# Optimization experiments

Measured on AMD Instinct MI355X. Metric: run time of the kernel, lower is better.

The kernel has to match this reference:

```python
import jax, jax.numpy as jnp
import numpy as np

FEAT_STRIDE = 16
PRE_NMS_TOP_N = 4000   # cfg[cfg_key].RPN_PRE_NMS_TOP_N
POST_NMS_TOP_N = 300   # cfg[cfg_key].RPN_POST_NMS_TOP_N
NMS_THRESH = 0.7       # cfg[cfg_key].RPN_NMS_THRESH


def _generate_anchors(base_size=16, ratios=(0.5, 1.0, 2.0), scales=(8, 16, 32)):
    ratios = np.array(ratios, dtype=np.float64)
    scales = np.array(scales, dtype=np.float64)
    base = np.array([1, 1, base_size, base_size], dtype=np.float64) - 1

    def whctrs(a):
        w = a[2] - a[0] + 1
        h = a[3] - a[1] + 1
        return w, h, a[0] + 0.5 * (w - 1), a[1] + 0.5 * (h - 1)

    def mk(ws, hs, xc, yc):
        ws = np.atleast_1d(ws)[:, None]
        hs = np.atleast_1d(hs)[:, None]
        return np.hstack((xc - 0.5 * (ws - 1), yc - 0.5 * (hs - 1),
                          xc + 0.5 * (ws - 1), yc + 0.5 * (hs - 1)))

    w, h, xc, yc = whctrs(base)
    size = w * h
    ws = np.round(np.sqrt(size / ratios))
    hs = np.round(ws * ratios)
    ratio_anchors = mk(ws, hs, xc, yc)
    out = []
    for i in range(ratio_anchors.shape[0]):
        w, h, xc, yc = whctrs(ratio_anchors[i])
        out.append(mk(w * scales, h * scales, xc, yc))
    return np.vstack(out).astype(np.float32)  # [9,4]


def _nms_keep(boxes, thresh):
    # boxes sorted by score desc, [N,4]; torchvision-style IoU (no +1).
    x1, y1, x2, y2 = boxes[:, 0], boxes[:, 1], boxes[:, 2], boxes[:, 3]
    areas = (x2 - x1) * (y2 - y1)
    lt = jnp.maximum(boxes[:, None, :2], boxes[None, :, :2])
    rb = jnp.minimum(boxes[:, None, 2:], boxes[None, :, 2:])
    wh = jnp.clip(rb - lt, 0.0)
    inter = wh[..., 0] * wh[..., 1]
    iou = inter / (areas[:, None] + areas[None, :] - inter + 1e-9)  # [N,N]
    N = boxes.shape[0]
    idx = jnp.arange(N)
    def body(i, keep):
        sup = (iou[i] > thresh) & (idx > i) & keep[i]
        return keep & ~sup
    return jax.lax.fori_loop(0, N, body, jnp.ones((N,), jnp.bool_))


def _per_image(boxes, scores):
    # pre-NMS top-k by score (matches sort-desc + slice)
    _, order = jax.lax.top_k(scores, PRE_NMS_TOP_N)
    b = boxes[order]
    keep = _nms_keep(jax.lax.stop_gradient(b), NMS_THRESH)
    rank = jnp.cumsum(keep) - 1                       # position among kept
    tgt = jnp.where(keep, rank, POST_NMS_TOP_N)       # OOB indices are dropped
    return jnp.zeros((POST_NMS_TOP_N, 4), boxes.dtype).at[tgt].set(b, mode='drop')


def reference(scores, bbox_deltas, im_info, anchors):
    B, A, H, W = scores.shape
    # anchor shifts over the feature grid
    sx = jnp.arange(W, dtype=scores.dtype) * FEAT_STRIDE
    sy = jnp.arange(H, dtype=scores.dtype) * FEAT_STRIDE
    yy, xx = jnp.meshgrid(sy, sx, indexing='ij')
    shifts = jnp.stack([xx.ravel(), yy.ravel(), xx.ravel(), yy.ravel()], axis=1)  # [K,4]
    all_anchors = (anchors[None, :, :] + shifts[:, None, :]).reshape(-1, 4)       # [K*A,4]

    deltas = bbox_deltas.transpose(0, 2, 3, 1).reshape(B, -1, 4)  # [B,K*A,4]
    sc = scores.transpose(0, 2, 3, 1).reshape(B, -1)              # [B,K*A]

    # bbox_transform_inv
    w = all_anchors[:, 2] - all_anchors[:, 0] + 1.0
    h = all_anchors[:, 3] - all_anchors[:, 1] + 1.0
    cx = all_anchors[:, 0] + 0.5 * w
    cy = all_anchors[:, 1] + 0.5 * h
    pcx = deltas[..., 0] * w + cx
    pcy = deltas[..., 1] * h + cy
    pw = jnp.exp(deltas[..., 2]) * w
    ph = jnp.exp(deltas[..., 3]) * h
    props = jnp.stack([pcx - 0.5 * pw, pcy - 0.5 * ph,
                       pcx + 0.5 * pw, pcy + 0.5 * ph], axis=-1)  # [B,K*A,4]

    # clip_boxes: x in [0, im_w-1], y in [0, im_h-1]
    hi = jnp.stack([im_info[:, 1] - 1, im_info[:, 0] - 1,
                    im_info[:, 1] - 1, im_info[:, 0] - 1], axis=1)  # [B,4]
    props = jnp.clip(props, 0.0, hi[:, None, :])

    boxes_out = jax.vmap(_per_image)(props, sc)  # [B,POST,4]
    batch_col = jnp.broadcast_to(
        jnp.arange(B, dtype=scores.dtype)[:, None, None], (B, POST_NMS_TOP_N, 1))
    return jnp.concatenate([batch_col, boxes_out], axis=-1)  # [B,POST,5]


def setup_inputs():
    key = jax.random.key(0)
    k1, k2 = jax.random.split(key)
    B, A, H, W = 4, 9, 50, 76
    scores = jax.random.normal(k1, (B, A, H, W), jnp.float32)
    bbox_deltas = jax.random.normal(k2, (B, 4 * A, H, W), jnp.float32) * 0.2
    im_info = jnp.tile(jnp.array([[800.0, 1216.0, 1.0]], jnp.float32), (B, 1))
    anchors = jnp.asarray(_generate_anchors())
    return {"scores": scores, "bbox_deltas": bbox_deltas,
            "im_info": im_info, "anchors": anchors}
```

## Files before the change

kernel.cpp:

```cpp
#include <hip/hip_runtime.h>
#include <stdint.h>

#define A_N 9
#define H_N 50
#define W_N 76
#define HW_N (H_N * W_N)
#define N_PROP (A_N * HW_N)
#define B_N 4
#define PRE_NMS 4000
#define POST_NMS 300
#define NMS_TH 0.7f
#define SORT_N 4096
#define MASK_WORDS 64
#define CAND_MAX 5120
#define NBINS 4096
#define NPAIR 32
#define NLW 5

__global__ __launch_bounds__(1024) void front_kernel(
    const float* __restrict__ scores,
    const float* __restrict__ deltas,
    const float* __restrict__ im_info,
    const float* __restrict__ anchors,
    float4* __restrict__ boxes,
    unsigned long long* __restrict__ keys,
    unsigned* __restrict__ cnt,
    unsigned long long* __restrict__ cand) {
#pragma clang fp contract(off)
    __shared__ unsigned hist[NBINS];
    __shared__ int Tlds;
    __shared__ unsigned cntL;
    const int b = blockIdx.x;
    const int tid = threadIdx.x;

    for (int i = tid; i < NBINS; i += 1024) hist[i] = 0u;
    if (tid == 0) cntL = 0u;
    __syncthreads();

    const float xhi = im_info[b * 3 + 1] - 1.0f;
    const float yhi = im_info[b * 3 + 0] - 1.0f;
    for (int it = 0; it < (N_PROP + 1023) / 1024; ++it) {
        int r = it * 1024 + tid;
        if (r < N_PROP) {
            int a = r / HW_N;
            int hw = r - a * HW_N;
            int hy = hw / W_N;
            int wx = hw - hy * W_N;

            float sx = (float)wx * 16.0f;
            float sy = (float)hy * 16.0f;
            float ax1 = anchors[a * 4 + 0] + sx;
            float ay1 = anchors[a * 4 + 1] + sy;
            float ax2 = anchors[a * 4 + 2] + sx;
            float ay2 = anchors[a * 4 + 3] + sy;
            float aw = ax2 - ax1 + 1.0f;
            float ah = ay2 - ay1 + 1.0f;
            float cx = ax1 + 0.5f * aw;
            float cy = ay1 + 0.5f * ah;

            const float* db = deltas + ((size_t)b * 36 + (size_t)a * 4) * HW_N + hw;
            float d0 = db[0];
            float d1 = db[HW_N];
            float d2 = db[2 * HW_N];
            float d3 = db[3 * HW_N];

            float pcx = d0 * aw + cx;
            float pcy = d1 * ah + cy;
            float pw  = expf(d2) * aw;
            float ph  = expf(d3) * ah;

            float x1 = pcx - 0.5f * pw;
            float y1 = pcy - 0.5f * ph;
            float x2 = pcx + 0.5f * pw;
            float y2 = pcy + 0.5f * ph;

            x1 = fminf(fmaxf(x1, 0.0f), xhi);
            y1 = fminf(fmaxf(y1, 0.0f), yhi);
            x2 = fminf(fmaxf(x2, 0.0f), xhi);
            y2 = fminf(fmaxf(y2, 0.0f), yhi);

            boxes[(size_t)b * N_PROP + r] = make_float4(x1, y1, x2, y2);

            float s = scores[((size_t)b * A_N + a) * HW_N + hw];
            unsigned f = __float_as_uint(s);
            unsigned sk = f ^ ((f & 0x80000000u) ? 0xFFFFFFFFu : 0x80000000u);
            unsigned n_ref = (unsigned)(hw * A_N + a);
            unsigned long long key =
                ((unsigned long long)sk << 32) | (unsigned)(~n_ref);
            keys[(size_t)b * N_PROP + r] = key;
            atomicAdd(&hist[(unsigned)(key >> 52)], 1u);
        }
    }
    __syncthreads();

    if (tid < 64) {
        int lane = tid;
        unsigned gsum = 0;
        for (int j = 0; j < 64; ++j) gsum += hist[lane * 64 + j];
        unsigned s = gsum;
        for (int d = 1; d < 64; d <<= 1) {
            unsigned t = (unsigned)__shfl_down((int)s, d);
            if (lane + d < 64) s += t;
        }
        unsigned long long bal = __ballot(s >= PRE_NMS);
        int gstar = 63 - __builtin_clzll(bal);
        unsigned after = (gstar < 63)
            ? (unsigned)__builtin_amdgcn_readlane((int)s, gstar + 1) : 0u;
        unsigned R = PRE_NMS - after;
        unsigned s2 = hist[gstar * 64 + lane];
        for (int d = 1; d < 64; d <<= 1) {
            unsigned t = (unsigned)__shfl_down((int)s2, d);
            if (lane + d < 64) s2 += t;
        }
        unsigned long long bal2 = __ballot(s2 >= R);
        int j = 63 - __builtin_clzll(bal2);
        if (lane == 0) Tlds = gstar * 64 + j;
    }
    __syncthreads();

    const int Tb = Tlds;
    for (int it = 0; it < (N_PROP + 1023) / 1024; ++it) {
        int n = it * 1024 + tid;
        bool pred = false;
        unsigned long long k = 0ull;
        if (n < N_PROP) {
            k = keys[(size_t)b * N_PROP + n];
            pred = ((int)(unsigned)(k >> 52) >= Tb);
        }
        unsigned long long m = __ballot(pred);
        if (m) {
            int lane = tid & 63;
            int lead = __ffsll((unsigned long long)m) - 1;
            unsigned base = 0;
            if (lane == lead) base = atomicAdd(&cntL, (unsigned)__popcll(m));
            base = __shfl((int)base, lead);
            if (pred) {
                unsigned pos = base + (unsigned)__popcll(m & ((1ull << lane) - 1ull));
                if (pos < CAND_MAX) cand[(size_t)b * CAND_MAX + pos] = k;
            }
        }
    }
    __syncthreads();
    if (tid == 0) cnt[b] = cntL;
}

__global__ __launch_bounds__(256) void rank_scatter_kernel(
    const unsigned long long* __restrict__ cand,
    const unsigned* __restrict__ cnt,
    const float4* __restrict__ boxes,
    float4* __restrict__ sortedBoxes) {
    __shared__ unsigned long long sk[256];
    int b = blockIdx.y;
    int tid = threadIdx.x;
    int ci = blockIdx.x * 64 + (tid >> 2);
    int q = tid & 3;
    int mc = (int)min(cnt[b], (unsigned)CAND_MAX);
    unsigned long long my = (ci < mc) ? cand[(size_t)b * CAND_MAX + ci] : 0ull;
    int rank = 0;
    int nt = (mc + 255) >> 8;
    for (int t = 0; t < nt; ++t) {
        int j = t * 256 + tid;
        sk[tid] = (j < mc) ? cand[(size_t)b * CAND_MAX + j] : 0ull;
        __syncthreads();
#pragma unroll 16
        for (int c = 0; c < 64; ++c) {
            int cc = q * 64 + ((c + q * 17) & 63);
            rank += (sk[cc] > my) ? 1 : 0;
        }
        __syncthreads();
    }
    rank += __shfl_xor(rank, 1);
    rank += __shfl_xor(rank, 2);
    if (q == 0 && ci < mc && rank < PRE_NMS) {
        unsigned n_ref = ~(unsigned)(my & 0xFFFFFFFFull);
        unsigned a = n_ref % A_N;
        unsigned hw = n_ref / A_N;
        sortedBoxes[(size_t)b * SORT_N + rank] =
            boxes[(size_t)b * N_PROP + a * HW_N + hw];
    }
    if (q == 1) {
        int pi = blockIdx.x * 64 + (tid >> 2);
        if (pi >= PRE_NMS && pi < SORT_N)
            sortedBoxes[(size_t)b * SORT_N + pi] = make_float4(0.f, 0.f, 0.f, 0.f);
    }
}

__global__ __launch_bounds__(256) void iou_mask_kernel(
    const float4* __restrict__ sortedBoxes,
    unsigned long long* __restrict__ colmaj,
    unsigned long long* __restrict__ rowmaj) {
#pragma clang fp contract(off)
    int b = blockIdx.y;
    int wv = threadIdx.x >> 6;
    int t = threadIdx.x & 63;
    int k = blockIdx.x * 4 + wv;
    int rc = 0;
    while (k >= 64 - rc) { k -= 64 - rc; ++rc; }
    int cc = rc + k;

    __shared__ float4 colb[4][64];
    colb[wv][t] = sortedBoxes[(size_t)b * SORT_N + cc * 64 + t];
    __syncthreads();

    int r = rc * 64 + t;
    float4 rb = sortedBoxes[(size_t)b * SORT_N + r];
    float rarea = (rb.z - rb.x) * (rb.w - rb.y);
    unsigned long long word = 0ull;
    for (int c = 0; c < 64; ++c) {
        int j = cc * 64 + c;
        float4 cb = colb[wv][c];
        float carea = (cb.z - cb.x) * (cb.w - cb.y);
        float ltx = fmaxf(rb.x, cb.x);
        float lty = fmaxf(rb.y, cb.y);
        float rbx = fminf(rb.z, cb.z);
        float rby = fminf(rb.w, cb.w);
        float iw = fmaxf(rbx - ltx, 0.0f);
        float ih = fmaxf(rby - lty, 0.0f);
        float inter = iw * ih;
        float iou = inter / (rarea + carea - inter + 1e-9f);
        if (iou > NMS_TH && j > r) word |= (1ull << c);
    }
    colmaj[((size_t)b * MASK_WORDS + cc) * SORT_N + r] = word;
    rowmaj[((size_t)b * SORT_N + r) * MASK_WORDS + cc] = word;
}

__device__ __forceinline__ unsigned long long rl64(unsigned long long v, int src) {
    unsigned lo = (unsigned)__builtin_amdgcn_readlane((int)(unsigned)(v & 0xFFFFFFFFull), src);
    unsigned hi = (unsigned)__builtin_amdgcn_readlane((int)(unsigned)(v >> 32), src);
    return ((unsigned long long)hi << 32) | lo;
}

__device__ __forceinline__ unsigned long long redor64(unsigned long long alive,
                                                      unsigned long long v, int lane) {
    unsigned long long x = ((alive >> lane) & 1ull) ? v : 0ull;
    x |= __shfl_xor(x, 1);
    x |= __shfl_xor(x, 2);
    x |= __shfl_xor(x, 4);
    x |= __shfl_xor(x, 8);
    x |= __shfl_xor(x, 16);
    x |= __shfl_xor(x, 32);
    return x;
}

__device__ __forceinline__ void block_sync() {
    asm volatile("s_waitcnt lgkmcnt(0)" ::: "memory");
    __builtin_amdgcn_s_barrier();
    asm volatile("" ::: "memory");
}

#define GLOAD(dst, addr) \
    asm volatile("global_load_dwordx2 %0, %1, off" : "=v"(dst) : "v"(addr))
#define WAITV0 asm volatile("s_waitcnt vmcnt(0)" ::: "memory")
#define SCHED0 __builtin_amdgcn_sched_barrier(0)

#define TILE_COL(P, t) ((t) < 6 ? 2 * (P) + (t) : 2 * (P) + 1 + ((t) - 6))
#define TILE_RB(P, t)  ((size_t)((t) < 6 ? 2 * (P) : 2 * (P) + 1) << 6)
#define TILE_ADDR(P, t) \
    (C + (size_t)(TILE_COL(P, t) < 64 ? TILE_COL(P, t) : 63) * SORT_N + TILE_RB(P, t) + lane)

#define ISSUE_PAIR(P)                                                          \
    do {                                                                       \
        pf_vmask = 0u;                                                         \
        GLOAD(pf0,  TILE_ADDR(P, 0));  if (TILE_COL(P, 0)  < 64) pf_vmask |= 1u << 0;  \
        GLOAD(pf1,  TILE_ADDR(P, 1));  if (TILE_COL(P, 1)  < 64) pf_vmask |= 1u << 1;  \
        GLOAD(pf2,  TILE_ADDR(P, 2));  if (TILE_COL(P, 2)  < 64) pf_vmask |= 1u << 2;  \
        GLOAD(pf3,  TILE_ADDR(P, 3));  if (TILE_COL(P, 3)  < 64) pf_vmask |= 1u << 3;  \
        GLOAD(pf4,  TILE_ADDR(P, 4));  if (TILE_COL(P, 4)  < 64) pf_vmask |= 1u << 4;  \
        GLOAD(pf5,  TILE_ADDR(P, 5));  if (TILE_COL(P, 5)  < 64) pf_vmask |= 1u << 5;  \
        GLOAD(pf6,  TILE_ADDR(P, 6));  if (TILE_COL(P, 6)  < 64) pf_vmask |= 1u << 6;  \
        GLOAD(pf7,  TILE_ADDR(P, 7));  if (TILE_COL(P, 7)  < 64) pf_vmask |= 1u << 7;  \
        GLOAD(pf8,  TILE_ADDR(P, 8));  if (TILE_COL(P, 8)  < 64) pf_vmask |= 1u << 8;  \
        GLOAD(pf9,  TILE_ADDR(P, 9));  if (TILE_COL(P, 9)  < 64) pf_vmask |= 1u << 9;  \
        GLOAD(pf10, TILE_ADDR(P, 10)); if (TILE_COL(P, 10) < 64) pf_vmask |= 1u << 10; \
    } while (0)

#define NEXTROW2(rk)                                                           \
    int rk;                                                                    \
    {                                                                          \
        if (xA) { int bb_ = __builtin_ctzll(xA); xA &= xA - 1; rk = baseA + bb_; } \
        else if (xB) { int bb_ = __builtin_ctzll(xB); xB &= xB - 1; rk = baseB + bb_; } \
        else rk = rpad;                                                        \
    }

__global__ __launch_bounds__(512, 1) void nms_scan_kernel(
    const unsigned long long* __restrict__ colmaj,
    const unsigned long long* __restrict__ rowmaj,
    const float4* __restrict__ sortedBoxes,
    float* __restrict__ out) {
    int b = blockIdx.x;
    int tid = threadIdx.x;
    int lane = tid & 63;
    int wv = tid >> 6;
    const unsigned long long* C = colmaj + (size_t)b * MASK_WORDS * SORT_N;
    const unsigned long long* R = rowmaj + (size_t)b * SORT_N * MASK_WORDS;

    __shared__ int kept[POST_NMS];
    __shared__ unsigned remW[MASK_WORDS][2];
    __shared__ unsigned long long aliveLds[MASK_WORDS];
    __shared__ unsigned long long ring[4][11][64];
    __shared__ unsigned long long car2[2][2];
    __shared__ int doneLds;
    __shared__ int kcntLds;

    if (tid < MASK_WORDS) { remW[tid][0] = 0u; remW[tid][1] = 0u; aliveLds[tid] = 0ull; }
    if (tid < 4) car2[tid >> 1][tid & 1] = 0ull;
    if (tid == 0) { doneLds = 0; kcntLds = 0; }

    unsigned long long pf0=0,pf1=0,pf2=0,pf3=0,pf4=0,pf5=0,pf6=0,pf7=0,pf8=0,pf9=0,pf10=0;
    unsigned pf_vmask = 0u;
    bool pf_have = false;
    unsigned long long gp0=0,gp1=0,gp2=0,gp3=0,gp4=0,gp5=0,gp6=0,gp7=0;
    bool ld_valid = false;

    if (wv == 1) {
        for (int t = 0; t < 11; ++t) {
            int col = TILE_COL(0, t);
            unsigned long long v =
                (col < 64) ? C[(size_t)col * SORT_N + TILE_RB(0, t) + lane] : 0ull;
            ring[0][t][lane] = v;
        }
        ISSUE_PAIR(1);
        pf_have = true;
    }
    block_sync();

    unsigned long long carA = 0ull, carB = 0ull;
    int kcnt = 0;

    for (int q = 0; q < NPAIR; ++q) {
        if (wv == 0) {
            int A = 2 * q, Bg = A + 1, slot = q & 3;
            unsigned long long dA  = ring[slot][0][lane];
            unsigned long long tA1 = ring[slot][1][lane];
            unsigned long long tA2 = ring[slot][2][lane];
            unsigned long long tA3 = ring[slot][3][lane];
            unsigned long long dB  = ring[slot][6][lane];
            unsigned long long tB1 = ring[slot][7][lane];
            unsigned long long tB2 = ring[slot][8][lane];
            unsigned long long remA =
                ((unsigned long long)remW[A][1] << 32) | (unsigned long long)remW[A][0];
            unsigned long long remB =
                ((unsigned long long)remW[Bg][1] << 32) | (unsigned long long)remW[Bg][0];
            unsigned long long h2A = car2[q & 1][0];
            unsigned long long h2B = car2[q & 1][1];
            bool hit = false;
            unsigned long long aliveA = 0ull, aliveB = 0ull;
            unsigned long long pend = ~(remA | carA | h2A);
            while (pend) {
                int bit = __builtin_ctzll(pend);
                if (lane == 0) kept[kcnt] = (A << 6) + bit;
                ++kcnt;
                aliveA |= 1ull << bit;
                if (kcnt == POST_NMS) { hit = true; break; }
                pend &= ~(rl64(dA, bit) | (1ull << bit));
            }
            if (!hit) {
                unsigned long long nA1 = redor64(aliveA, tA1, lane);
                pend = ~(remB | carB | h2B | nA1);
                while (pend) {
                    int bit = __builtin_ctzll(pend);
                    if (lane == 0) kept[kcnt] = (Bg << 6) + bit;
                    ++kcnt;
                    aliveB |= 1ull << bit;
                    if (kcnt == POST_NMS) { hit = true; break; }
                    pend &= ~(rl64(dB, bit) | (1ull << bit));
                }
            }
            carA = redor64(aliveA, tA2, lane) | redor64(aliveB, tB1, lane);
            carB = redor64(aliveA, tA3, lane) | redor64(aliveB, tB2, lane);
            if (lane == 0) {
                aliveLds[A]  = aliveA;
                aliveLds[Bg] = aliveB;
                kcntLds = kcnt;
                if (hit) doneLds = 1;
            }
        } else if (wv == 1) {
            if (pf_have) {
                WAITV0;
                SCHED0;
                int wp = q + 1;
                if (wp < NPAIR) {
                    int ws = wp & 3;
                    ring[ws][0][lane]  = (pf_vmask & (1u << 0))  ? pf0  : 0ull;
                    ring[ws][1][lane]  = (pf_vmask & (1u << 1))  ? pf1  : 0ull;
                    ring[ws][2][lane]  = (pf_vmask & (1u << 2))  ? pf2  : 0ull;
                    ring[ws][3][lane]  = (pf_vmask & (1u << 3))  ? pf3  : 0ull;
                    ring[ws][4][lane]  = (pf_vmask & (1u << 4))  ? pf4  : 0ull;
                    ring[ws][5][lane]  = (pf_vmask & (1u << 5))  ? pf5  : 0ull;
                    ring[ws][6][lane]  = (pf_vmask & (1u << 6))  ? pf6  : 0ull;
                    ring[ws][7][lane]  = (pf_vmask & (1u << 7))  ? pf7  : 0ull;
                    ring[ws][8][lane]  = (pf_vmask & (1u << 8))  ? pf8  : 0ull;
                    ring[ws][9][lane]  = (pf_vmask & (1u << 9))  ? pf9  : 0ull;
                    ring[ws][10][lane] = (pf_vmask & (1u << 10)) ? pf10 : 0ull;
                }
                pf_have = false;
            }
            int ip = q + 2;
            if (ip < NPAIR) {
                ISSUE_PAIR(ip);
                pf_have = true;
            }
        } else if (wv == 2) {
            if (q >= 1) {
                int p = q - 1, sp = p & 3;
                unsigned long long aA = aliveLds[2 * p];
                unsigned long long aB = aliveLds[2 * p + 1];
                unsigned long long tA4 = ring[sp][4][lane];
                unsigned long long tA5 = ring[sp][5][lane];
                unsigned long long tB3 = ring[sp][9][lane];
                unsigned long long tB4 = ring[sp][10][lane];
                unsigned long long c0 = redor64(aA, tA4, lane) | redor64(aB, tB3, lane);
                unsigned long long c1 = redor64(aA, tA5, lane) | redor64(aB, tB4, lane);
                if (lane == 0) {
                    car2[(q + 1) & 1][0] = c0;
                    car2[(q + 1) & 1][1] = c1;
                }
            }
        } else {
            if (ld_valid) {
                WAITV0;
                SCHED0;
                unsigned long long acc =
                    ((gp0 | gp1) | (gp2 | gp3)) | ((gp4 | gp5) | (gp6 | gp7));
                unsigned lo = (unsigned)acc, hi = (unsigned)(acc >> 32);
                if (lo) atomicOr(&remW[lane][0], lo);
                if (hi) atomicOr(&remW[lane][1], hi);
                ld_valid = false;
            }
            if (q >= 1) {
                int p = q - 1, gA = 2 * p, gB = 2 * p + 1;
                unsigned long long aA = aliveLds[gA];
                unsigned long long aB = aliveLds[gB];
                int k = wv - 3;
                unsigned long long below = (1ull << lane) - 1ull;
                bool inA = (aA >> lane) & 1ull;
                bool inB = (aB >> lane) & 1ull;
                int posA = (int)__popcll(aA & below);
                int posB = (int)__popcll(aA) + (int)__popcll(aB & below);
                unsigned long long mA = __ballot(inA && (posA % NLW) == k);
                unsigned long long mB = __ballot(inB && (posB % NLW) == k);
                if (mA | mB) {
                    int baseA = gA << 6, baseB = gB << 6;
                    unsigned long long xA = mA, xB = mB;
                    int rpad = mA ? (baseA + __builtin_ctzll(mA))
                                  : (baseB + __builtin_ctzll(mB));
                    NEXTROW2(r0) NEXTROW2(r1) NEXTROW2(r2) NEXTROW2(r3)
                    NEXTROW2(r4) NEXTROW2(r5) NEXTROW2(r6) NEXTROW2(r7)
                    const unsigned long long* Rb = R + lane;
                    GLOAD(gp0, Rb + (size_t)r0 * MASK_WORDS);
                    GLOAD(gp1, Rb + (size_t)r1 * MASK_WORDS);
                    GLOAD(gp2, Rb + (size_t)r2 * MASK_WORDS);
                    GLOAD(gp3, Rb + (size_t)r3 * MASK_WORDS);
                    GLOAD(gp4, Rb + (size_t)r4 * MASK_WORDS);
                    GLOAD(gp5, Rb + (size_t)r5 * MASK_WORDS);
                    GLOAD(gp6, Rb + (size_t)r6 * MASK_WORDS);
                    GLOAD(gp7, Rb + (size_t)r7 * MASK_WORDS);
                    ld_valid = true;
                    unsigned long long ovf = 0ull;
                    while (xA) {
                        int bb = __builtin_ctzll(xA); xA &= xA - 1;
                        ovf |= Rb[(size_t)(baseA + bb) * MASK_WORDS];
                    }
                    while (xB) {
                        int bb = __builtin_ctzll(xB); xB &= xB - 1;
                        ovf |= Rb[(size_t)(baseB + bb) * MASK_WORDS];
                    }
                    if (ovf) {
                        unsigned lo = (unsigned)ovf, hi = (unsigned)(ovf >> 32);
                        if (lo) atomicOr(&remW[lane][0], lo);
                        if (hi) atomicOr(&remW[lane][1], hi);
                    }
                }
            }
        }
        block_sync();
        if (doneLds) break;
    }

    WAITV0;
    __syncthreads();

    int kc = kcntLds;
    for (int r = tid; r < POST_NMS; r += 512) {
        float* o = out + ((size_t)b * POST_NMS + r) * 5;
        float4 bx = make_float4(0.f, 0.f, 0.f, 0.f);
        if (r < kc) bx = sortedBoxes[(size_t)b * SORT_N + kept[r]];
        o[0] = (float)b;
        o[1] = bx.x;
        o[2] = bx.y;
        o[3] = bx.z;
        o[4] = bx.w;
    }
}

extern "C" void kernel_launch(void* const* d_in, const int* in_sizes, int n_in,
                              void* d_out, int out_size, void* d_ws, size_t ws_size,
                              hipStream_t stream) {
    const float* scores  = (const float*)d_in[0];
    const float* deltas  = (const float*)d_in[1];
    const float* im_info = (const float*)d_in[2];
    const float* anchors = (const float*)d_in[3];
    float* out = (float*)d_out;

    char* ws = (char*)d_ws;
    size_t off = 0;
    float4* boxes = (float4*)(ws + off);
    off += (size_t)B_N * N_PROP * sizeof(float4);
    off = (off + 255) & ~(size_t)255;
    unsigned long long* keys = (unsigned long long*)(ws + off);
    off += (size_t)B_N * N_PROP * sizeof(unsigned long long);
    off = (off + 255) & ~(size_t)255;
    float4* sortedBoxes = (float4*)(ws + off);
    off += (size_t)B_N * SORT_N * sizeof(float4);
    off = (off + 255) & ~(size_t)255;
    unsigned long long* colmaj = (unsigned long long*)(ws + off);
    off += (size_t)B_N * MASK_WORDS * SORT_N * sizeof(unsigned long long);
    off = (off + 255) & ~(size_t)255;
    unsigned long long* rowmaj = (unsigned long long*)(ws + off);
    off += (size_t)B_N * SORT_N * MASK_WORDS * sizeof(unsigned long long);
    off = (off + 255) & ~(size_t)255;
    unsigned long long* cand = (unsigned long long*)(ws + off);
    off += (size_t)B_N * CAND_MAX * sizeof(unsigned long long);
    off = (off + 255) & ~(size_t)255;
    unsigned* cnt = (unsigned*)(ws + off);
    off += (size_t)B_N * sizeof(unsigned);

    front_kernel<<<B_N, 1024, 0, stream>>>(
        scores, deltas, im_info, anchors, boxes, keys, cnt, cand);
    rank_scatter_kernel<<<dim3(CAND_MAX / 64, B_N), 256, 0, stream>>>(
        cand, cnt, boxes, sortedBoxes);
    iou_mask_kernel<<<dim3(520, B_N), 256, 0, stream>>>(sortedBoxes, colmaj, rowmaj);
    nms_scan_kernel<<<B_N, 512, 0, stream>>>(colmaj, rowmaj, sortedBoxes, out);
}
```

Baseline: 219.9 us.

## Split box decode into wide grid kernel and replace shuffle OR-reductions with readlane loops

The fused front kernel ran the box decode and key generation on only one block per image. That work now runs in a separate decode kernel spread across many blocks, and a mid kernel rereads the keys to build the histogram. In the NMS scan, the shuffle-based OR reduction over alive rows is replaced by loops over set alive bits using scalar readlane, which costs work proportional to the number of kept boxes rather than a fixed shuffle tree. This adds a kernel launch and an extra global round trip for the keys, and the readlane loops may be slower when many rows are alive.

```diff
diff --git a/kernel.cpp b/kernel.cpp
--- a/kernel.cpp
+++ b/kernel.cpp
@@ -16,17 +16,74 @@
 #define NBINS 4096
 #define NPAIR 32
 #define NLW 5
-
-__global__ __launch_bounds__(1024) void front_kernel(
+#define DEC_BLKS ((N_PROP + 255) / 256)
+
+__global__ __launch_bounds__(256) void decode_kernel(
     const float* __restrict__ scores,
     const float* __restrict__ deltas,
     const float* __restrict__ im_info,
     const float* __restrict__ anchors,
     float4* __restrict__ boxes,
-    unsigned long long* __restrict__ keys,
+    unsigned long long* __restrict__ keys) {
+#pragma clang fp contract(off)
+    int tid = threadIdx.x;
+    int b = blockIdx.y;
+    int r = blockIdx.x * 256 + tid;
+    if (r >= N_PROP) return;
+
+    int a = r / HW_N;
+    int hw = r - a * HW_N;
+    int hy = hw / W_N;
+    int wx = hw - hy * W_N;
+
+    float sx = (float)wx * 16.0f;
+    float sy = (float)hy * 16.0f;
+    float ax1 = anchors[a * 4 + 0] + sx;
+    float ay1 = anchors[a * 4 + 1] + sy;
+    float ax2 = anchors[a * 4 + 2] + sx;
+    float ay2 = anchors[a * 4 + 3] + sy;
+    float aw = ax2 - ax1 + 1.0f;
+    float ah = ay2 - ay1 + 1.0f;
+    float cx = ax1 + 0.5f * aw;
+    float cy = ay1 + 0.5f * ah;
+
+    const float* db = deltas + ((size_t)b * 36 + (size_t)a * 4) * HW_N + hw;
+    float d0 = db[0];
+    float d1 = db[HW_N];
+    float d2 = db[2 * HW_N];
+    float d3 = db[3 * HW_N];
+
+    float pcx = d0 * aw + cx;
+    float pcy = d1 * ah + cy;
+    float pw  = expf(d2) * aw;
+    float ph  = expf(d3) * ah;
+
+    float x1 = pcx - 0.5f * pw;
+    float y1 = pcy - 0.5f * ph;
+    float x2 = pcx + 0.5f * pw;
+    float y2 = pcy + 0.5f * ph;
+
+    float xhi = im_info[b * 3 + 1] - 1.0f;
+    float yhi = im_info[b * 3 + 0] - 1.0f;
+    x1 = fminf(fmaxf(x1, 0.0f), xhi);
+    y1 = fminf(fmaxf(y1, 0.0f), yhi);
+    x2 = fminf(fmaxf(x2, 0.0f), xhi);
+    y2 = fminf(fmaxf(y2, 0.0f), yhi);
+
+    boxes[(size_t)b * N_PROP + r] = make_float4(x1, y1, x2, y2);
+
+    float s = scores[((size_t)b * A_N + a) * HW_N + hw];
+    unsigned f = __float_as_uint(s);
+    unsigned sk = f ^ ((f & 0x80000000u) ? 0xFFFFFFFFu : 0x80000000u);
+    unsigned n_ref = (unsigned)(hw * A_N + a);
+    unsigned long long key = ((unsigned long long)sk << 32) | (unsigned)(~n_ref);
+    keys[(size_t)b * N_PROP + r] = key;
+}
+
+__global__ __launch_bounds__(1024) void mid_kernel(
+    const unsigned long long* __restrict__ keys,
     unsigned* __restrict__ cnt,
     unsigned long long* __restrict__ cand) {
-#pragma clang fp contract(off)
     __shared__ unsigned hist[NBINS];
     __shared__ int Tlds;
     __shared__ unsigned cntL;
@@ -37,58 +94,11 @@
     if (tid == 0) cntL = 0u;
     __syncthreads();
 
-    const float xhi = im_info[b * 3 + 1] - 1.0f;
-    const float yhi = im_info[b * 3 + 0] - 1.0f;
     for (int it = 0; it < (N_PROP + 1023) / 1024; ++it) {
-        int r = it * 1024 + tid;
-        if (r < N_PROP) {
-            int a = r / HW_N;
-            int hw = r - a * HW_N;
-            int hy = hw / W_N;
-            int wx = hw - hy * W_N;
-
-            float sx = (float)wx * 16.0f;
-            float sy = (float)hy * 16.0f;
-            float ax1 = anchors[a * 4 + 0] + sx;
-            float ay1 = anchors[a * 4 + 1] + sy;
-            float ax2 = anchors[a * 4 + 2] + sx;
-            float ay2 = anchors[a * 4 + 3] + sy;
-            float aw = ax2 - ax1 + 1.0f;
-            float ah = ay2 - ay1 + 1.0f;
-            float cx = ax1 + 0.5f * aw;
-            float cy = ay1 + 0.5f * ah;
-
-            const float* db = deltas + ((size_t)b * 36 + (size_t)a * 4) * HW_N + hw;
-            float d0 = db[0];
-            float d1 = db[HW_N];
-            float d2 = db[2 * HW_N];
-            float d3 = db[3 * HW_N];
-
-            float pcx = d0 * aw + cx;
-            float pcy = d1 * ah + cy;
-            float pw  = expf(d2) * aw;
-            float ph  = expf(d3) * ah;
-
-            float x1 = pcx - 0.5f * pw;
-            float y1 = pcy - 0.5f * ph;
-            float x2 = pcx + 0.5f * pw;
-            float y2 = pcy + 0.5f * ph;
-
-            x1 = fminf(fmaxf(x1, 0.0f), xhi);
-            y1 = fminf(fmaxf(y1, 0.0f), yhi);
-            x2 = fminf(fmaxf(x2, 0.0f), xhi);
-            y2 = fminf(fmaxf(y2, 0.0f), yhi);
-
-            boxes[(size_t)b * N_PROP + r] = make_float4(x1, y1, x2, y2);
-
-            float s = scores[((size_t)b * A_N + a) * HW_N + hw];
-            unsigned f = __float_as_uint(s);
-            unsigned sk = f ^ ((f & 0x80000000u) ? 0xFFFFFFFFu : 0x80000000u);
-            unsigned n_ref = (unsigned)(hw * A_N + a);
-            unsigned long long key =
-                ((unsigned long long)sk << 32) | (unsigned)(~n_ref);
-            keys[(size_t)b * N_PROP + r] = key;
-            atomicAdd(&hist[(unsigned)(key >> 52)], 1u);
+        int n = it * 1024 + tid;
+        if (n < N_PROP) {
+            unsigned long long k = keys[(size_t)b * N_PROP + n];
+            atomicAdd(&hist[(unsigned)(k >> 52)], 1u);
         }
     }
     __syncthreads();
@@ -228,18 +238,6 @@
     unsigned lo = (unsigned)__builtin_amdgcn_readlane((int)(unsigned)(v & 0xFFFFFFFFull), src);
     unsigned hi = (unsigned)__builtin_amdgcn_readlane((int)(unsigned)(v >> 32), src);
     return ((unsigned long long)hi << 32) | lo;
-}
-
-__device__ __forceinline__ unsigned long long redor64(unsigned long long alive,
-                                                      unsigned long long v, int lane) {
-    unsigned long long x = ((alive >> lane) & 1ull) ? v : 0ull;
-    x |= __shfl_xor(x, 1);
-    x |= __shfl_xor(x, 2);
-    x |= __shfl_xor(x, 4);
-    x |= __shfl_xor(x, 8);
-    x |= __shfl_xor(x, 16);
-    x |= __shfl_xor(x, 32);
-    return x;
 }
 
 __device__ __forceinline__ void block_sync() {
@@ -354,8 +352,16 @@
                 if (kcnt == POST_NMS) { hit = true; break; }
                 pend &= ~(rl64(dA, bit) | (1ull << bit));
             }
+            unsigned long long ncA = 0ull, ncB = 0ull;
             if (!hit) {
-                unsigned long long nA1 = redor64(aliveA, tA1, lane);
+                unsigned long long nA1 = 0ull;
+                unsigned long long am = aliveA;
+                while (am) {
+                    int i = __builtin_ctzll(am); am &= am - 1;
+                    nA1 |= rl64(tA1, i);
+                    ncA |= rl64(tA2, i);
+                    ncB |= rl64(tA3, i);
+                }
                 pend = ~(remB | carB | h2B | nA1);
                 while (pend) {
                     int bit = __builtin_ctzll(pend);
@@ -365,9 +371,15 @@
                     if (kcnt == POST_NMS) { hit = true; break; }
                     pend &= ~(rl64(dB, bit) | (1ull << bit));
                 }
-            }
-            carA = redor64(aliveA, tA2, lane) | redor64(aliveB, tB1, lane);
-            carB = redor64(aliveA, tA3, lane) | redor64(aliveB, tB2, lane);
+                am = aliveB;
+                while (am) {
+                    int i = __builtin_ctzll(am); am &= am - 1;
+                    ncA |= rl64(tB1, i);
+                    ncB |= rl64(tB2, i);
+                }
+            }
+            carA = ncA;
+            carB = ncB;
             if (lane == 0) {
                 aliveLds[A]  = aliveA;
                 aliveLds[Bg] = aliveB;
@@ -409,8 +421,19 @@
                 unsigned long long tA5 = ring[sp][5][lane];
                 unsigned long long tB3 = ring[sp][9][lane];
                 unsigned long long tB4 = ring[sp][10][lane];
-                unsigned long long c0 = redor64(aA, tA4, lane) | redor64(aB, tB3, lane);
-                unsigned long long c1 = redor64(aA, tA5, lane) | redor64(aB, tB4, lane);
+                unsigned long long c0 = 0ull, c1 = 0ull;
+                unsigned long long am = aA;
+                while (am) {
+                    int i = __builtin_ctzll(am); am &= am - 1;
+                    c0 |= rl64(tA4, i);
+                    c1 |= rl64(tA5, i);
+                }
+                am = aB;
+                while (am) {
+                    int i = __builtin_ctzll(am); am &= am - 1;
+                    c0 |= rl64(tB3, i);
+                    c1 |= rl64(tB4, i);
+                }
                 if (lane == 0) {
                     car2[(q + 1) & 1][0] = c0;
                     car2[(q + 1) & 1][1] = c1;
@@ -525,8 +548,9 @@
     unsigned* cnt = (unsigned*)(ws + off);
     off += (size_t)B_N * sizeof(unsigned);
 
-    front_kernel<<<B_N, 1024, 0, stream>>>(
-        scores, deltas, im_info, anchors, boxes, keys, cnt, cand);
+    decode_kernel<<<dim3(DEC_BLKS, B_N), 256, 0, stream>>>(
+        scores, deltas, im_info, anchors, boxes, keys);
+    mid_kernel<<<B_N, 1024, 0, stream>>>(keys, cnt, cand);
     rank_scatter_kernel<<<dim3(CAND_MAX / 64, B_N), 256, 0, stream>>>(
         cand, cnt, boxes, sortedBoxes);
     iou_mask_kernel<<<dim3(520, B_N), 256, 0, stream>>>(sortedBoxes, colmaj, rowmaj);
```

After: 222.8 us. No clear change (+1.3%).

## Split box decoding into a wide grid kernel separate from histogram selection

Applied to the files above, without the earlier changes.

Box decoding and key generation move out of the 4-block front kernel into a new kernel launched over many 256-thread blocks per image, so the whole GPU takes part instead of four workgroups. The histogram/threshold stage becomes its own kernel that rereads the keys from global memory. The cost is an extra kernel launch and a second pass over the key array, in exchange for much more parallelism in the decode stage.

```diff
diff --git a/kernel.cpp b/kernel.cpp
--- a/kernel.cpp
+++ b/kernel.cpp
@@ -16,17 +16,74 @@
 #define NBINS 4096
 #define NPAIR 32
 #define NLW 5
-
-__global__ __launch_bounds__(1024) void front_kernel(
+#define DEC_BLKS ((N_PROP + 255) / 256)
+
+__global__ __launch_bounds__(256) void decode_kernel(
     const float* __restrict__ scores,
     const float* __restrict__ deltas,
     const float* __restrict__ im_info,
     const float* __restrict__ anchors,
     float4* __restrict__ boxes,
-    unsigned long long* __restrict__ keys,
+    unsigned long long* __restrict__ keys) {
+#pragma clang fp contract(off)
+    int tid = threadIdx.x;
+    int b = blockIdx.y;
+    int r = blockIdx.x * 256 + tid;
+    if (r >= N_PROP) return;
+
+    int a = r / HW_N;
+    int hw = r - a * HW_N;
+    int hy = hw / W_N;
+    int wx = hw - hy * W_N;
+
+    float sx = (float)wx * 16.0f;
+    float sy = (float)hy * 16.0f;
+    float ax1 = anchors[a * 4 + 0] + sx;
+    float ay1 = anchors[a * 4 + 1] + sy;
+    float ax2 = anchors[a * 4 + 2] + sx;
+    float ay2 = anchors[a * 4 + 3] + sy;
+    float aw = ax2 - ax1 + 1.0f;
+    float ah = ay2 - ay1 + 1.0f;
+    float cx = ax1 + 0.5f * aw;
+    float cy = ay1 + 0.5f * ah;
+
+    const float* db = deltas + ((size_t)b * 36 + (size_t)a * 4) * HW_N + hw;
+    float d0 = db[0];
+    float d1 = db[HW_N];
+    float d2 = db[2 * HW_N];
+    float d3 = db[3 * HW_N];
+
+    float pcx = d0 * aw + cx;
+    float pcy = d1 * ah + cy;
+    float pw  = expf(d2) * aw;
+    float ph  = expf(d3) * ah;
+
+    float x1 = pcx - 0.5f * pw;
+    float y1 = pcy - 0.5f * ph;
+    float x2 = pcx + 0.5f * pw;
+    float y2 = pcy + 0.5f * ph;
+
+    float xhi = im_info[b * 3 + 1] - 1.0f;
+    float yhi = im_info[b * 3 + 0] - 1.0f;
+    x1 = fminf(fmaxf(x1, 0.0f), xhi);
+    y1 = fminf(fmaxf(y1, 0.0f), yhi);
+    x2 = fminf(fmaxf(x2, 0.0f), xhi);
+    y2 = fminf(fmaxf(y2, 0.0f), yhi);
+
+    boxes[(size_t)b * N_PROP + r] = make_float4(x1, y1, x2, y2);
+
+    float s = scores[((size_t)b * A_N + a) * HW_N + hw];
+    unsigned f = __float_as_uint(s);
+    unsigned sk = f ^ ((f & 0x80000000u) ? 0xFFFFFFFFu : 0x80000000u);
+    unsigned n_ref = (unsigned)(hw * A_N + a);
+    unsigned long long key = ((unsigned long long)sk << 32) | (unsigned)(~n_ref);
+    keys[(size_t)b * N_PROP + r] = key;
+}
+
+__global__ __launch_bounds__(1024) void mid_kernel(
+    const unsigned long long* __restrict__ keys,
     unsigned* __restrict__ cnt,
     unsigned long long* __restrict__ cand) {
-#pragma clang fp contract(off)
     __shared__ unsigned hist[NBINS];
     __shared__ int Tlds;
     __shared__ unsigned cntL;
@@ -37,58 +94,11 @@
     if (tid == 0) cntL = 0u;
     __syncthreads();
 
-    const float xhi = im_info[b * 3 + 1] - 1.0f;
-    const float yhi = im_info[b * 3 + 0] - 1.0f;
     for (int it = 0; it < (N_PROP + 1023) / 1024; ++it) {
-        int r = it * 1024 + tid;
-        if (r < N_PROP) {
-            int a = r / HW_N;
-            int hw = r - a * HW_N;
-            int hy = hw / W_N;
-            int wx = hw - hy * W_N;
-
-            float sx = (float)wx * 16.0f;
-            float sy = (float)hy * 16.0f;
-            float ax1 = anchors[a * 4 + 0] + sx;
-            float ay1 = anchors[a * 4 + 1] + sy;
-            float ax2 = anchors[a * 4 + 2] + sx;
-            float ay2 = anchors[a * 4 + 3] + sy;
-            float aw = ax2 - ax1 + 1.0f;
-            float ah = ay2 - ay1 + 1.0f;
-            float cx = ax1 + 0.5f * aw;
-            float cy = ay1 + 0.5f * ah;
-
-            const float* db = deltas + ((size_t)b * 36 + (size_t)a * 4) * HW_N + hw;
-            float d0 = db[0];
-            float d1 = db[HW_N];
-            float d2 = db[2 * HW_N];
-            float d3 = db[3 * HW_N];
-
-            float pcx = d0 * aw + cx;
-            float pcy = d1 * ah + cy;
-            float pw  = expf(d2) * aw;
-            float ph  = expf(d3) * ah;
-
-            float x1 = pcx - 0.5f * pw;
-            float y1 = pcy - 0.5f * ph;
-            float x2 = pcx + 0.5f * pw;
-            float y2 = pcy + 0.5f * ph;
-
-            x1 = fminf(fmaxf(x1, 0.0f), xhi);
-            y1 = fminf(fmaxf(y1, 0.0f), yhi);
-            x2 = fminf(fmaxf(x2, 0.0f), xhi);
-            y2 = fminf(fmaxf(y2, 0.0f), yhi);
-
-            boxes[(size_t)b * N_PROP + r] = make_float4(x1, y1, x2, y2);
-
-            float s = scores[((size_t)b * A_N + a) * HW_N + hw];
-            unsigned f = __float_as_uint(s);
-            unsigned sk = f ^ ((f & 0x80000000u) ? 0xFFFFFFFFu : 0x80000000u);
-            unsigned n_ref = (unsigned)(hw * A_N + a);
-            unsigned long long key =
-                ((unsigned long long)sk << 32) | (unsigned)(~n_ref);
-            keys[(size_t)b * N_PROP + r] = key;
-            atomicAdd(&hist[(unsigned)(key >> 52)], 1u);
+        int n = it * 1024 + tid;
+        if (n < N_PROP) {
+            unsigned long long k = keys[(size_t)b * N_PROP + n];
+            atomicAdd(&hist[(unsigned)(k >> 52)], 1u);
         }
     }
     __syncthreads();
@@ -525,8 +535,9 @@
     unsigned* cnt = (unsigned*)(ws + off);
     off += (size_t)B_N * sizeof(unsigned);
 
-    front_kernel<<<B_N, 1024, 0, stream>>>(
-        scores, deltas, im_info, anchors, boxes, keys, cnt, cand);
+    decode_kernel<<<dim3(DEC_BLKS, B_N), 256, 0, stream>>>(
+        scores, deltas, im_info, anchors, boxes, keys);
+    mid_kernel<<<B_N, 1024, 0, stream>>>(keys, cnt, cand);
     rank_scatter_kernel<<<dim3(CAND_MAX / 64, B_N), 256, 0, stream>>>(
         cand, cnt, boxes, sortedBoxes);
     iou_mask_kernel<<<dim3(520, B_N), 256, 0, stream>>>(sortedBoxes, colmaj, rowmaj);
```

Result: faster. 203.5 us (-7.5%).
